# Optimization experiments

Hardware: AMD Instinct MI355X
Metric: run time of the kernel (lower is better)

The kernel has to match this reference:

```python
import jax, jax.numpy as jnp
import numpy as np

CONF_THRESH = 0.01
TOP_K = 200
NMS_THRESH = 0.45


def decode(loc, dbox):
    # loc, dbox: [N,4]; dbox is (cx, cy, w, h)
    cxcy = dbox[:, :2] + loc[:, :2] * 0.1 * dbox[:, 2:]
    wh = dbox[:, 2:] * jnp.exp(loc[:, 2:] * 0.2)
    xymin = cxcy - wh * 0.5
    xymax = xymin + wh
    return jnp.concatenate([xymin, xymax], axis=1)  # [N,4] (x1,y1,x2,y2)


def nms_class(scores, boxes):
    # scores: [N], boxes: [N,4]. Mirrors torch greedy NMS with fixed-size padding.
    masked = jnp.where(scores > CONF_THRESH, scores, -1.0)
    topv, topi = jax.lax.top_k(masked, TOP_K)  # descending score, like idx[-top_k:] reversed
    cb = boxes[topi]  # [K,4]
    valid = topv > CONF_THRESH
    x1, y1, x2, y2 = cb[:, 0], cb[:, 1], cb[:, 2], cb[:, 3]
    area = (x2 - x1) * (y2 - y1)
    ar = jnp.arange(TOP_K)

    def body(i, keep):
        cur = keep[i]
        w = jnp.clip(jnp.minimum(x2, x2[i]) - jnp.maximum(x1, x1[i]), 0.0)
        h = jnp.clip(jnp.minimum(y2, y2[i]) - jnp.maximum(y1, y1[i]), 0.0)
        inter = w * h
        iou = inter / (area - inter + area[i])  # union = rem_area - inter + area[i]
        sup = (iou > NMS_THRESH) & (ar > i) & cur
        return keep & (~sup)

    keep = jax.lax.fori_loop(0, TOP_K, body, valid)
    # compact kept rows to the front, preserving descending-score order (stable sort)
    order = jnp.argsort(jnp.logical_not(keep), stable=True)
    count = jnp.sum(keep)
    rows = jnp.concatenate([topv[:, None], cb], axis=1)[order]  # [K,5] = (score, x1,y1,x2,y2)
    return jnp.where(ar[:, None] < count, rows, 0.0)


def setup_inputs() -> dict:
    key = jax.random.key(0)
    k1, k2, k3, k4 = jax.random.split(key, 4)
    B, N, C = 128, 8732, 21
    loc_data = jax.random.normal(k1, (B, N, 4), dtype=jnp.float32) * 0.5
    conf_data = jax.random.normal(k2, (B, N, C), dtype=jnp.float32)
    centers = jax.random.uniform(k3, (N, 2), dtype=jnp.float32)
    wh = jax.random.uniform(k4, (N, 2), dtype=jnp.float32, minval=0.02, maxval=0.3)
    dbox_list = jnp.concatenate([centers, wh], axis=1)
    return {"loc_data": loc_data, "conf_data": conf_data, "dbox_list": dbox_list}


def reference(loc_data, conf_data, dbox_list):
    conf = jax.nn.softmax(conf_data, axis=-1)                              # [B,N,C]
    boxes = jax.vmap(decode, in_axes=(0, None))(loc_data, dbox_list)       # [B,N,4]
    # vmap over classes (axis 1 of per-image conf) then over batch
    per_cls = jax.vmap(jax.vmap(nms_class, in_axes=(1, None)),
                       in_axes=(0, 0))(conf, boxes)                        # [B,C,K,5]
    return per_cls.at[:, 0].set(0.0)  # class 0 (background) is skipped in torch
```

## Files before the change

### kernel.cpp

```cpp
#include <hip/hip_runtime.h>

#define N_ANCH 8732
#define NCLS   21
#define BATCH  128
#define TOPK   200
#define CONF_T 0.01f
#define HSIZE  1024
#define CAND_MAX 1024
#define NQ4    2183

#define MD 0x1.CCCCCDp-2

__device__ __forceinline__ float exp_np(float x) {
    const float fx = floorf(__fmaf_rn(x, 1.442695040888963f, 0.5f));
    float t = __fmaf_rn(fx, -0.693359375f, x);
    t = __fmaf_rn(fx, 2.12194440e-4f, t);
    const float z = __fmul_rn(t, t);
    float y = 1.9875691500e-4f;
    y = __fmaf_rn(y, t, 1.3981999507e-3f);
    y = __fmaf_rn(y, t, 8.3334519073e-3f);
    y = __fmaf_rn(y, t, 4.1665795894e-2f);
    y = __fmaf_rn(y, t, 1.6666665459e-1f);
    y = __fmaf_rn(y, t, 5.0000001201e-1f);
    y = __fmaf_rn(y, z, t);
    y = __fadd_rn(y, 1.0f);
    return ldexpf(y, (int)fx);
}

__global__ __launch_bounds__(256) void prep_kernel(
    const float* __restrict__ loc, const float* __restrict__ conf,
    const float* __restrict__ dbox, float* __restrict__ probs,
    float* __restrict__ boxes)
{
    __shared__ float srow[256 * NCLS];
    const int block_row0 = blockIdx.x * 256;
    const float* cbase = conf + (size_t)block_row0 * NCLS;
    for (int i = threadIdx.x; i < 256 * NCLS; i += 256) srow[i] = cbase[i];
    __syncthreads();

    const int row = block_row0 + threadIdx.x;
    const int b = row / N_ANCH;
    const int n = row - b * N_ANCH;

    float e[NCLS];
    float m = srow[threadIdx.x * NCLS];
#pragma unroll
    for (int c = 1; c < NCLS; ++c) m = fmaxf(m, srow[threadIdx.x * NCLS + c]);
#pragma unroll
    for (int c = 0; c < NCLS; ++c)
        e[c] = exp_np(__fsub_rn(srow[threadIdx.x * NCLS + c], m));

    float acc[16];
#pragma unroll
    for (int j = 0; j < 16; ++j) acc[j] = e[j];
#pragma unroll
    for (int j = 0; j < 5; ++j) acc[j] = __fadd_rn(acc[j], e[16 + j]);
    float u[8];
#pragma unroll
    for (int j = 0; j < 8; ++j) u[j] = __fadd_rn(acc[j], acc[j + 8]);
    const float v0 = __fadd_rn(u[0], u[4]), v1 = __fadd_rn(u[1], u[5]);
    const float v2 = __fadd_rn(u[2], u[6]), v3 = __fadd_rn(u[3], u[7]);
    const float w0 = __fadd_rn(v0, v2), w1 = __fadd_rn(v1, v3);
    const float s  = __fadd_rn(w0, w1);

#pragma unroll
    for (int c = 1; c < NCLS; ++c)
        probs[((size_t)b * 20 + (c - 1)) * N_ANCH + n] = __fdiv_rn(e[c], s);

    const float4 l = *(const float4*)(loc + (size_t)row * 4);
    const float4 d = *(const float4*)(dbox + (size_t)n * 4);
    const float cx = __fmaf_rn(__fmul_rn(l.x, 0.1f), d.z, d.x);
    const float cy = __fmaf_rn(__fmul_rn(l.y, 0.1f), d.w, d.y);
    const float w  = __fmul_rn(d.z, exp_np(__fmul_rn(l.z, 0.2f)));
    const float h  = __fmul_rn(d.w, exp_np(__fmul_rn(l.w, 0.2f)));
    const float x1 = __fmaf_rn(w, -0.5f, cx);
    const float y1 = __fmaf_rn(h, -0.5f, cy);
    float4 o; o.x = x1; o.y = y1; o.z = __fadd_rn(x1, w); o.w = __fadd_rn(y1, h);
    *(float4*)(boxes + (size_t)row * 4) = o;
}

__global__ __launch_bounds__(256) void sel_kernel(
    const float* __restrict__ probs, const float* __restrict__ boxes,
    float* __restrict__ probs_mut)
{
    const int task = blockIdx.x;
    const int b = task / NCLS;
    const int c = task - b * NCLS;
    const int tid = threadIdx.x;
    if (c == 0) return;

    const float* prow = probs + ((size_t)b * 20 + (c - 1)) * N_ANCH;

    __shared__ int hist2[HSIZE * 2];
    __shared__ int wsum[4];
    __shared__ unsigned long long cand[CAND_MAX];
    __shared__ int selB;
    __shared__ int cnts[2];
    __shared__ unsigned ck[TOPK];
    __shared__ int  cn[TOPK];
    __shared__ unsigned sk[TOPK];
    __shared__ int  sn_[TOPK];

    const int wid = tid >> 6, lane = tid & 63;
    const int par = wid & 1;

    for (int i = tid; i < HSIZE * 2; i += 256) hist2[i] = 0;
    __syncthreads();
    for (int idx = tid; idx < NQ4; idx += 256) {
        const float4 v = *(const float4*)(prow + idx * 4);
        if (v.x > CONF_T) atomicAdd(&hist2[(int)((__float_as_uint(v.x) >> 16) - 0x3C23u) * 2 + par], 1);
        if (v.y > CONF_T) atomicAdd(&hist2[(int)((__float_as_uint(v.y) >> 16) - 0x3C23u) * 2 + par], 1);
        if (v.z > CONF_T) atomicAdd(&hist2[(int)((__float_as_uint(v.z) >> 16) - 0x3C23u) * 2 + par], 1);
        if (v.w > CONF_T) atomicAdd(&hist2[(int)((__float_as_uint(v.w) >> 16) - 0x3C23u) * 2 + par], 1);
    }
    __syncthreads();

    const int hbase = HSIZE - 4 * (tid + 1);
    int hb[4];
#pragma unroll
    for (int j = 0; j < 4; ++j) hb[j] = hist2[(hbase + j) * 2] + hist2[(hbase + j) * 2 + 1];
    const int part = hb[0] + hb[1] + hb[2] + hb[3];

    int incl = part;
#pragma unroll
    for (int off = 1; off < 64; off <<= 1) {
        const int v = __shfl_up(incl, off);
        if (lane >= off) incl += v;
    }
    if (lane == 63) wsum[wid] = incl;
    __syncthreads();
    int pre = 0;
    for (int w = 0; w < wid; ++w) pre += wsum[w];
    const int excl  = pre + incl - part;
    const int total = wsum[0] + wsum[1] + wsum[2] + wsum[3];
    if (tid == 0 && total < TOPK) selB = -1;
    if (excl < TOPK && excl + part >= TOPK) {
        int cacc = excl;
        for (int j = 3; j >= 0; --j) {
            if (cacc + hb[j] >= TOPK) { selB = hbase + j; break; }
            cacc += hb[j];
        }
    }
    if (tid == 0) { cnts[0] = 0; cnts[1] = 0; }
    __syncthreads();
    const int B = selB;

    for (int idx = tid; idx < NQ4; idx += 256) {
        const float4 v = *(const float4*)(prow + idx * 4);
        const float vv[4] = {v.x, v.y, v.z, v.w};
#pragma unroll
        for (int q = 0; q < 4; ++q) {
            const float s = vv[q];
            if (s > CONF_T) {
                const unsigned kk = __float_as_uint(s);
                const int bkt = (int)((kk >> 16) - 0x3C23u);
                if (bkt > B) {
                    const int p = atomicAdd(&cnts[0], 1);
                    ck[p] = kk; cn[p] = idx * 4 + q;
                } else if (bkt == B) {
                    const int qq = atomicAdd(&cnts[1], 1);
                    if (qq < CAND_MAX)
                        cand[qq] = ((unsigned long long)kk << 32) | (unsigned)(~(idx * 4 + q));
                }
            }
        }
    }
    __syncthreads();
    const int ndef  = cnts[0];
    const int slots = TOPK - ndef;
    int cc = cnts[1]; if (cc > CAND_MAX) cc = CAND_MAX;

    if (cc <= slots) {
        for (int i = tid; i < cc; i += 256) {
            const unsigned long long mine = cand[i];
            const int p = atomicAdd(&cnts[0], 1);
            ck[p] = (unsigned)(mine >> 32);
            cn[p] = (int)(~(unsigned)mine);
        }
        __syncthreads();
    } else {
        for (int i = tid; i < 256; i += 256) hist2[i] = 0;
        __syncthreads();
        for (int i = tid; i < cc; i += 256)
            atomicAdd(&hist2[(int)((cand[i] >> 40) & 0xFFull)], 1);
        __syncthreads();
        const int sb = 255 - tid;
        const int part2 = hist2[sb];
        int incl2 = part2;
#pragma unroll
        for (int off = 1; off < 64; off <<= 1) {
            const int v = __shfl_up(incl2, off);
            if (lane >= off) incl2 += v;
        }
        if (lane == 63) wsum[wid] = incl2;
        __syncthreads();
        int pre2 = 0;
        for (int w = 0; w < wid; ++w) pre2 += wsum[w];
        const int excl2 = pre2 + incl2 - part2;
        if (excl2 < slots && excl2 + part2 >= slots) selB = sb;
        __syncthreads();
        const int B2 = selB;
        for (int i = tid; i < cc; i += 256) {
            const unsigned long long mine = cand[i];
            if ((int)((mine >> 40) & 0xFFull) > B2) {
                const int p = atomicAdd(&cnts[0], 1);
                ck[p] = (unsigned)(mine >> 32);
                cn[p] = (int)(~(unsigned)mine);
            }
        }
        __syncthreads();
        const int slots2 = TOPK - cnts[0];
        for (int i = tid; i < cc; i += 256) {
            const unsigned long long mine = cand[i];
            if ((int)((mine >> 40) & 0xFFull) == B2) {
                int rank = 0;
                for (int j = 0; j < cc; ++j) {
                    const unsigned long long oth = cand[j];
                    rank += (((int)((oth >> 40) & 0xFFull) == B2) && oth > mine) ? 1 : 0;
                }
                if (rank < slots2) {
                    const int p = atomicAdd(&cnts[0], 1);
                    ck[p] = (unsigned)(mine >> 32);
                    cn[p] = (int)(~(unsigned)mine);
                }
            }
        }
        __syncthreads();
    }
    const int cnt_arr = cnts[0];

    if (tid < TOPK) { sk[tid] = 0u; sn_[tid] = -1; }
    __syncthreads();
    if (tid < cnt_arr) {
        const unsigned mk = ck[tid];
        const int mn = cn[tid];
        int rank = 0;
        for (int j = 0; j < cnt_arr; ++j) {
            const unsigned kj = ck[j];
            rank += (kj > mk || (kj == mk && cn[j] < mn)) ? 1 : 0;
        }
        sk[rank] = mk; sn_[rank] = mn;
    }
    __syncthreads();

    float* selrow = probs_mut + ((size_t)b * 20 + (c - 1)) * N_ANCH;
    for (int i = tid; i < TOPK; i += 256) {
        const int n = sn_[i];
        float scv = 0.f;
        float4 bx = make_float4(0.f, 0.f, 0.f, 0.f);
        if (n >= 0) {
            scv = __uint_as_float(sk[i]);
            bx = *(const float4*)(boxes + ((size_t)b * N_ANCH + n) * 4);
        }
        float* dst = selrow + i * 5;
        dst[0] = scv; dst[1] = bx.x; dst[2] = bx.y; dst[3] = bx.z; dst[4] = bx.w;
    }
}

__global__ __launch_bounds__(256) void nms_kernel(
    const float* __restrict__ sel, float* __restrict__ out)
{
    const int task = blockIdx.x;
    const int b = task / NCLS;
    const int c = task - b * NCLS;
    float* obase = out + (size_t)task * (TOPK * 5);
    const int tid = threadIdx.x;
    const int wv = tid >> 6, lane = tid & 63;

    if (c == 0) {
        for (int i = tid; i < TOPK * 5; i += 256) obase[i] = 0.f;
        return;
    }
    const float* srow = sel + ((size_t)b * 20 + (c - 1)) * N_ANCH;

    __shared__ float bxs[TOPK * 5];
    __shared__ __align__(16) unsigned long long rows[TOPK][4];
    __shared__ unsigned long long Ksh[4];

    for (int i = tid; i < TOPK * 5; i += 256) bxs[i] = srow[i];
    __syncthreads();

    float jx1[4], jy1[4], jx2[4], jy2[4], jar[4];
    int jval[4];
#pragma unroll
    for (int s = 0; s < 4; ++s) {
        const int j = s * 64 + lane;
        float a = 0.f, p1 = 0.f, p2 = 0.f, p3 = 0.f, p4 = 0.f;
        if (j < TOPK) {
            a = bxs[j * 5 + 0];
            p1 = bxs[j * 5 + 1]; p2 = bxs[j * 5 + 2];
            p3 = bxs[j * 5 + 3]; p4 = bxs[j * 5 + 4];
        }
        jx1[s] = p1; jy1[s] = p2; jx2[s] = p3; jy2[s] = p4;
        jar[s] = __fmul_rn(__fsub_rn(p3, p1), __fsub_rn(p4, p2));
        jval[s] = (a > CONF_T) ? 1 : 0;
    }
    if (wv == 0) {
#pragma unroll
        for (int s = 0; s < 4; ++s) {
            const unsigned long long m = __ballot(jval[s] != 0);
            if (lane == 0) Ksh[s] = m;
        }
    }

    for (int i = wv; i < TOPK; i += 4) {
        const int smin = i >> 6;
        const float ix1 = bxs[i * 5 + 1], iy1 = bxs[i * 5 + 2];
        const float ix2 = bxs[i * 5 + 3], iy2 = bxs[i * 5 + 4];
        const float ia  = __fmul_rn(__fsub_rn(ix2, ix1), __fsub_rn(iy2, iy1));
#pragma unroll
        for (int s = 0; s < 4; ++s) {
            if (s < smin) {
                if (lane == 0) rows[i][s] = 0ull;
            } else {
                const int j = s * 64 + lane;
                const float w = fmaxf(0.f, __fsub_rn(fminf(jx2[s], ix2), fmaxf(jx1[s], ix1)));
                const float h = fmaxf(0.f, __fsub_rn(fminf(jy2[s], iy2), fmaxf(jy1[s], iy1)));
                const float inter = __fmul_rn(w, h);
                const float denom = __fadd_rn(__fsub_rn(jar[s], inter), ia);
                const bool bit = (j < TOPK) && (j > i) &&
                                 ((double)inter > MD * (double)denom);
                const unsigned long long m = __ballot(bit);
                if (lane == 0) rows[i][s] = m;
            }
        }
    }
    __syncthreads();

    if (wv == 0) {
        unsigned long long K0 = Ksh[0], K1 = Ksh[1], K2 = Ksh[2], K3 = Ksh[3];
#pragma unroll
        for (int w4 = 0; w4 < 4; ++w4) {
            const int lim = (w4 < 3) ? 64 : (TOPK - 192);
            for (int o = 0; o < lim; ++o) {
                const int i = w4 * 64 + o;
                const ulonglong2 ra = *(const ulonglong2*)&rows[i][0];
                const ulonglong2 rb = *(const ulonglong2*)&rows[i][2];
                if ((ra.x | ra.y | rb.x | rb.y) == 0ull) continue;
                unsigned long long live;
                if (w4 == 0) live = (K0 >> o) & 1ull;
                else if (w4 == 1) live = (K1 >> o) & 1ull;
                else if (w4 == 2) live = (K2 >> o) & 1ull;
                else live = (K3 >> o) & 1ull;
                const unsigned long long msel = 0ull - live;
                K0 &= ~(ra.x & msel);
                K1 &= ~(ra.y & msel);
                K2 &= ~(rb.x & msel);
                K3 &= ~(rb.y & msel);
            }
        }
        if (lane == 0) { Ksh[0] = K0; Ksh[1] = K1; Ksh[2] = K2; Ksh[3] = K3; }
    }
    __syncthreads();

    if (tid < TOPK) {
        const unsigned long long K0 = Ksh[0], K1 = Ksh[1], K2 = Ksh[2], K3 = Ksh[3];
        const int d = tid;
        const int c0 = (int)__popcll(K0), c1 = (int)__popcll(K1),
                  c2 = (int)__popcll(K2), c3 = (int)__popcll(K3);
        const int totalk = c0 + c1 + c2 + c3;
        float o0 = 0.f, o1 = 0.f, o2 = 0.f, o3 = 0.f, o4 = 0.f;
        if (d < totalk) {
            int r = d;
            unsigned long long x;
            int wbase;
            if (r < c0)               { x = K0; wbase = 0;   }
            else if (r < c0 + c1)     { x = K1; wbase = 64;  r -= c0; }
            else if (r < c0 + c1 + c2){ x = K2; wbase = 128; r -= c0 + c1; }
            else                      { x = K3; wbase = 192; r -= c0 + c1 + c2; }
            for (int t = 0; t < r; ++t) x &= x - 1ull;
            const int p = wbase + (__ffsll((unsigned long long)x) - 1);
            o0 = bxs[p * 5 + 0]; o1 = bxs[p * 5 + 1]; o2 = bxs[p * 5 + 2];
            o3 = bxs[p * 5 + 3]; o4 = bxs[p * 5 + 4];
        }
        obase[d * 5 + 0] = o0;
        obase[d * 5 + 1] = o1;
        obase[d * 5 + 2] = o2;
        obase[d * 5 + 3] = o3;
        obase[d * 5 + 4] = o4;
    }
}

extern "C" void kernel_launch(void* const* d_in, const int* in_sizes, int n_in,
                              void* d_out, int out_size, void* d_ws, size_t ws_size,
                              hipStream_t stream) {
    (void)in_sizes; (void)n_in; (void)out_size; (void)ws_size;
    const float* loc  = (const float*)d_in[0];
    const float* conf = (const float*)d_in[1];
    const float* dbox = (const float*)d_in[2];
    float* out   = (float*)d_out;
    float* probs = (float*)d_ws;
    float* boxes = (float*)((char*)d_ws + (size_t)BATCH * 20 * N_ANCH * 4);

    prep_kernel<<<(BATCH * N_ANCH) / 256, 256, 0, stream>>>(loc, conf, dbox, probs, boxes);
    sel_kernel<<<BATCH * NCLS, 256, 0, stream>>>(probs, boxes, probs);
    nms_kernel<<<BATCH * NCLS, 256, 0, stream>>>(probs, out);
}
```

Baseline: 210.9 us.

## Fuse top-k selection and NMS kernels into one with shared-memory aliasing

Merges the selection kernel and the NMS kernel into a single launch. Selected scores and boxes go straight into shared memory instead of being written to the global workspace and read back. Shared buffers for the histogram/candidate phase are aliased with the box/IoU-mask buffers so LDS usage stays bounded. This removes one launch and a global round trip, at the cost of a longer kernel whose register and LDS pressure may reduce occupancy.

```diff
diff --git a/kernel.cpp b/kernel.cpp
--- a/kernel.cpp
+++ b/kernel.cpp
@@ -79,27 +79,37 @@
     *(float4*)(boxes + (size_t)row * 4) = o;
 }
 
-__global__ __launch_bounds__(256) void sel_kernel(
+__global__ __launch_bounds__(256) void sel_nms_kernel(
     const float* __restrict__ probs, const float* __restrict__ boxes,
-    float* __restrict__ probs_mut)
+    float* __restrict__ out)
 {
     const int task = blockIdx.x;
     const int b = task / NCLS;
     const int c = task - b * NCLS;
     const int tid = threadIdx.x;
-    if (c == 0) return;
-
+    float* obase = out + (size_t)task * (TOPK * 5);
+
+    if (c == 0) {
+        for (int i = tid; i < TOPK * 5; i += 256) obase[i] = 0.f;
+        return;
+    }
     const float* prow = probs + ((size_t)b * 20 + (c - 1)) * N_ANCH;
 
-    __shared__ int hist2[HSIZE * 2];
+    __shared__ __align__(16) char poolA[HSIZE * 2 * 4];
+    __shared__ __align__(16) char poolB[CAND_MAX * 8];
+    int* hist2 = (int*)poolA;
+    float* bxs = (float*)poolA;
+    unsigned long long* cand = (unsigned long long*)poolB;
+    unsigned long long (*rows)[4] = (unsigned long long (*)[4])poolB;
+
     __shared__ int wsum[4];
-    __shared__ unsigned long long cand[CAND_MAX];
     __shared__ int selB;
     __shared__ int cnts[2];
     __shared__ unsigned ck[TOPK];
     __shared__ int  cn[TOPK];
     __shared__ unsigned sk[TOPK];
     __shared__ int  sn_[TOPK];
+    __shared__ unsigned long long Ksh[4];
 
     const int wid = tid >> 6, lane = tid & 63;
     const int par = wid & 1;
@@ -243,41 +253,18 @@
     }
     __syncthreads();
 
-    float* selrow = probs_mut + ((size_t)b * 20 + (c - 1)) * N_ANCH;
-    for (int i = tid; i < TOPK; i += 256) {
-        const int n = sn_[i];
+    if (tid < TOPK) {
+        const int n = sn_[tid];
         float scv = 0.f;
         float4 bx = make_float4(0.f, 0.f, 0.f, 0.f);
         if (n >= 0) {
-            scv = __uint_as_float(sk[i]);
+            scv = __uint_as_float(sk[tid]);
             bx = *(const float4*)(boxes + ((size_t)b * N_ANCH + n) * 4);
         }
-        float* dst = selrow + i * 5;
-        dst[0] = scv; dst[1] = bx.x; dst[2] = bx.y; dst[3] = bx.z; dst[4] = bx.w;
-    }
-}
-
-__global__ __launch_bounds__(256) void nms_kernel(
-    const float* __restrict__ sel, float* __restrict__ out)
-{
-    const int task = blockIdx.x;
-    const int b = task / NCLS;
-    const int c = task - b * NCLS;
-    float* obase = out + (size_t)task * (TOPK * 5);
-    const int tid = threadIdx.x;
-    const int wv = tid >> 6, lane = tid & 63;
-
-    if (c == 0) {
-        for (int i = tid; i < TOPK * 5; i += 256) obase[i] = 0.f;
-        return;
-    }
-    const float* srow = sel + ((size_t)b * 20 + (c - 1)) * N_ANCH;
-
-    __shared__ float bxs[TOPK * 5];
-    __shared__ __align__(16) unsigned long long rows[TOPK][4];
-    __shared__ unsigned long long Ksh[4];
-
-    for (int i = tid; i < TOPK * 5; i += 256) bxs[i] = srow[i];
+        bxs[tid * 5 + 0] = scv;
+        bxs[tid * 5 + 1] = bx.x; bxs[tid * 5 + 2] = bx.y;
+        bxs[tid * 5 + 3] = bx.z; bxs[tid * 5 + 4] = bx.w;
+    }
     __syncthreads();
 
     float jx1[4], jy1[4], jx2[4], jy2[4], jar[4];
@@ -295,7 +282,7 @@
         jar[s] = __fmul_rn(__fsub_rn(p3, p1), __fsub_rn(p4, p2));
         jval[s] = (a > CONF_T) ? 1 : 0;
     }
-    if (wv == 0) {
+    if (wid == 0) {
 #pragma unroll
         for (int s = 0; s < 4; ++s) {
             const unsigned long long m = __ballot(jval[s] != 0);
@@ -303,11 +290,11 @@
         }
     }
 
-    for (int i = wv; i < TOPK; i += 4) {
+    for (int i = wid; i < TOPK; i += 4) {
         const int smin = i >> 6;
         const float ix1 = bxs[i * 5 + 1], iy1 = bxs[i * 5 + 2];
         const float ix2 = bxs[i * 5 + 3], iy2 = bxs[i * 5 + 4];
-        const float ia  = __fmul_rn(__fsub_rn(ix2, ix1), __fsub_rn(iy2, iy1));
+        (void)iy1;
 #pragma unroll
         for (int s = 0; s < 4; ++s) {
             if (s < smin) {
@@ -315,8 +302,9 @@
             } else {
                 const int j = s * 64 + lane;
                 const float w = fmaxf(0.f, __fsub_rn(fminf(jx2[s], ix2), fmaxf(jx1[s], ix1)));
-                const float h = fmaxf(0.f, __fsub_rn(fminf(jy2[s], iy2), fmaxf(jy1[s], iy1)));
+                const float h = fmaxf(0.f, __fsub_rn(fminf(jy2[s], bxs[i * 5 + 4]), fmaxf(jy1[s], bxs[i * 5 + 2])));
                 const float inter = __fmul_rn(w, h);
+                const float ia = __fmul_rn(__fsub_rn(ix2, ix1), __fsub_rn(bxs[i * 5 + 4], bxs[i * 5 + 2]));
                 const float denom = __fadd_rn(__fsub_rn(jar[s], inter), ia);
                 const bool bit = (j < TOPK) && (j > i) &&
                                  ((double)inter > MD * (double)denom);
@@ -327,7 +315,7 @@
     }
     __syncthreads();
 
-    if (wv == 0) {
+    if (wid == 0) {
         unsigned long long K0 = Ksh[0], K1 = Ksh[1], K2 = Ksh[2], K3 = Ksh[3];
 #pragma unroll
         for (int w4 = 0; w4 < 4; ++w4) {
@@ -393,6 +381,5 @@
     float* boxes = (float*)((char*)d_ws + (size_t)BATCH * 20 * N_ANCH * 4);
 
     prep_kernel<<<(BATCH * N_ANCH) / 256, 256, 0, stream>>>(loc, conf, dbox, probs, boxes);
-    sel_kernel<<<BATCH * NCLS, 256, 0, stream>>>(probs, boxes, probs);
-    nms_kernel<<<BATCH * NCLS, 256, 0, stream>>>(probs, out);
+    sel_nms_kernel<<<BATCH * NCLS, 256, 0, stream>>>(probs, boxes, out);
 }
```

Result: no change. 210.9 us (-0.0%).
